# Performance work log

Measured on AMD Instinct MI355X. Metric: run time of the kernel, lower is better.

## Reference

```python
import jax, jax.numpy as jnp
import numpy as np


def _gcn_conv(h, src, dst, W, b, n):
    # PyG GCNConv: x @ W, then symmetric-normalized aggregation with self-loops
    deg = jax.ops.segment_sum(jnp.ones(src.shape[0], h.dtype), dst, num_segments=n)
    dinv = jax.lax.rsqrt(jnp.maximum(deg, 1.0))  # deg >= 1 because self-loops are included
    norm = dinv[src] * dinv[dst]                 # [E]
    m = (h @ W)[src] * norm[:, None]             # gather + scale
    return jax.ops.segment_sum(m, dst, num_segments=n) + b


def setup_inputs() -> dict:
    key = jax.random.key(0)
    N, E, F, H, L, V = 50000, 800000, 128, 256, 64, 128
    ks = jax.random.split(key, 16)
    s = lambda fan_in: 1.0 / np.sqrt(fan_in)
    return {
        "x": jax.random.randint(ks[0], (N,), 0, V),
        "edge_index": jax.random.randint(ks[1], (2, E), 0, N),
        "eps": jax.random.normal(ks[2], (N, L), jnp.float32),
        "emb": jax.random.normal(ks[3], (V, F), jnp.float32),
        "W1": jax.random.normal(ks[4], (F, H), jnp.float32) * s(F),
        "b1": jnp.zeros((H,), jnp.float32),
        "W2": jax.random.normal(ks[5], (H, H), jnp.float32) * s(H),
        "b2": jnp.zeros((H,), jnp.float32),
        "Wmu": jax.random.normal(ks[6], (H, L), jnp.float32) * s(H),
        "bmu": jnp.zeros((L,), jnp.float32),
        "Wlv": jax.random.normal(ks[7], (H, L), jnp.float32) * s(H),
        "blv": jnp.zeros((L,), jnp.float32),
        "W3": jax.random.normal(ks[8], (L, H), jnp.float32) * s(L),
        "b3": jnp.zeros((H,), jnp.float32),
        "W4": jax.random.normal(ks[9], (H, V), jnp.float32) * s(H),
        "b4": jnp.zeros((V,), jnp.float32),
        "Wcap": jax.random.normal(ks[10], (L, 1), jnp.float32) * s(L),
        "bcap": jnp.zeros((1,), jnp.float32),
    }


def reference(x, edge_index, eps, emb, W1, b1, W2, b2, Wmu, bmu, Wlv, blv, W3, b3, W4, b4, Wcap, bcap):
    n = x.shape[0]
    loops = jnp.arange(n, dtype=edge_index.dtype)
    src = jnp.concatenate([edge_index[0], loops])  # add self-loops once, reuse
    dst = jnp.concatenate([edge_index[1], loops])

    h = emb[x]                                      # [N, F] embedding lookup
    h = jax.nn.relu(_gcn_conv(h, src, dst, W1, b1, n))
    h = jax.nn.relu(_gcn_conv(h, src, dst, W2, b2, n))
    mu = h @ Wmu + bmu
    logvar = h @ Wlv + blv
    z = mu + eps * jnp.exp(0.5 * logvar)            # reparameterize
    recon_x = jax.nn.relu(z @ W3 + b3) @ W4 + b4    # decode
    capitalize = jax.nn.sigmoid(z @ Wcap + bcap)
    return recon_x, capitalize, mu, logvar
```

## Files before the change

### kernel.cpp

```cpp
#include <hip/hip_runtime.h>
#include <math.h>


typedef __attribute__((ext_vector_type(8))) short bf16x8;
typedef __attribute__((ext_vector_type(4))) float f32x4;

__device__ inline unsigned short f2bf(float x) {
    unsigned u = __float_as_uint(x);
    return (unsigned short)((u + 0x7FFFu + ((u >> 16) & 1u)) >> 16);
}
__device__ inline float bf2f(unsigned short h) {
    return __uint_as_float(((unsigned)h) << 16);
}

__global__ __launch_bounds__(256) void k_deg_count(const int* __restrict__ dst,
                                                   int* __restrict__ degint, int E) {
    int e = blockIdx.x * 256 + threadIdx.x;
    if (e < E) atomicAdd(&degint[dst[e]], 1);
}

#define SCAN_BLOCK 1024
__global__ __launch_bounds__(SCAN_BLOCK) void k_scan_local(
        const int* __restrict__ degint, int* __restrict__ row_ptr,
        int* __restrict__ bsum, float* __restrict__ dinv, int N) {
    __shared__ int s[SCAN_BLOCK];
    int gid = blockIdx.x * SCAN_BLOCK + threadIdx.x;
    int d = (gid < N) ? (degint[gid] + 1) : 0;
    if (gid < N) dinv[gid] = rsqrtf((float)d);
    s[threadIdx.x] = d;
    __syncthreads();
    for (int off = 1; off < SCAN_BLOCK; off <<= 1) {
        int t = (threadIdx.x >= off) ? s[threadIdx.x - off] : 0;
        __syncthreads();
        s[threadIdx.x] += t;
        __syncthreads();
    }
    if (gid < N) row_ptr[gid] = s[threadIdx.x] - d;
    if (threadIdx.x == SCAN_BLOCK - 1) bsum[blockIdx.x] = s[SCAN_BLOCK - 1];
}

__global__ void k_scan_bsum(int* __restrict__ bsum, int nb) {
    if (blockIdx.x == 0 && threadIdx.x == 0) {
        int acc = 0;
        for (int i = 0; i < nb; ++i) { int v = bsum[i]; bsum[i] = acc; acc += v; }
    }
}

__global__ __launch_bounds__(256) void k_scan_add(int* __restrict__ row_ptr,
                                                  const int* __restrict__ bsum,
                                                  int N, int T) {
    int gid = blockIdx.x * 256 + threadIdx.x;
    if (gid < N) row_ptr[gid] += bsum[gid / SCAN_BLOCK];
    if (gid == 0) row_ptr[N] = T;
}

__global__ __launch_bounds__(256) void k_fill(
        const int* __restrict__ src, const int* __restrict__ dst,
        const int* __restrict__ x, const float* __restrict__ dinv,
        const int* __restrict__ row_ptr, int* __restrict__ cursor,
        int4* __restrict__ pack, int E, int N) {
    const int base = (blockIdx.x * 256 + threadIdx.x) * 4;
#pragma unroll
    for (int j = 0; j < 4; ++j) {
        int e = base + j;
        if (e < E) {
            int s = src[e], d = dst[e];
            float w = dinv[s] * dinv[d];
            int pos = row_ptr[d] + atomicAdd(&cursor[d], 1);
            pack[pos] = make_int4(__float_as_int(w), x[s], s, 0);
        } else if (e < E + N) {
            int i = e - E;
            float di = dinv[i];
            int pos = row_ptr[i] + atomicAdd(&cursor[i], 1);
            pack[pos] = make_int4(__float_as_int(di * di), x[i], i, 0);
        }
    }
}

__global__ __launch_bounds__(256) void k_cvt_all(
        const float* __restrict__ B0, unsigned short* __restrict__ h0, int K0, int N0,
        const float* __restrict__ B1, unsigned short* __restrict__ h1, int K1, int N1,
        const float* __restrict__ B2, unsigned short* __restrict__ h2, int K2, int N2,
        const float* __restrict__ B3, unsigned short* __restrict__ h3, int K3, int N3,
        const float* __restrict__ B4, unsigned short* __restrict__ h4, int K4, int N4) {
    const float* B; unsigned short* Bh; int K, Ncol;
    switch (blockIdx.y) {
        case 0: B = B0; Bh = h0; K = K0; Ncol = N0; break;
        case 1: B = B1; Bh = h1; K = K1; Ncol = N1; break;
        case 2: B = B2; Bh = h2; K = K2; Ncol = N2; break;
        case 3: B = B3; Bh = h3; K = K3; Ncol = N3; break;
        default: B = B4; Bh = h4; K = K4; Ncol = N4; break;
    }
    int i = blockIdx.x * 256 + threadIdx.x;
    if (i >= K * Ncol) return;
    int k = i / Ncol, n = i - k * Ncol;
    Bh[(long)n * K + k] = f2bf(B[i]);
}

__global__ __launch_bounds__(256) void k_gemm_f32(
        const float* __restrict__ A, const float* __restrict__ B,
        unsigned short* __restrict__ Cb, int M, int K, int Ncol) {
    constexpr int BM = 64, BN = 64, BK = 16;
    __shared__ float As[BK][BM];
    __shared__ float Bs[BK][BN];
    const int tid = threadIdx.x;
    const int tx = tid & 15, ty = tid >> 4;
    const int rowBase = blockIdx.x * BM;
    const int colBase = blockIdx.y * BN;
    const int lr = tid >> 2, lc4 = tid & 3;
    const int br = tid >> 4, bc4 = tid & 15;
    const int arow = rowBase + lr;
    const int K4 = K >> 2, N4 = Ncol >> 2;
    const float4* A4 = (const float4*)A;
    const float4* B4 = (const float4*)B;
    float acc[4][4] = {{0.f}};
    for (int k0 = 0; k0 < K; k0 += BK) {
        float4 av = make_float4(0.f, 0.f, 0.f, 0.f);
        if (arow < M) av = A4[(long)arow * K4 + (k0 >> 2) + lc4];
        As[lc4 * 4 + 0][lr] = av.x;
        As[lc4 * 4 + 1][lr] = av.y;
        As[lc4 * 4 + 2][lr] = av.z;
        As[lc4 * 4 + 3][lr] = av.w;
        float4 bv = B4[(long)(k0 + br) * N4 + (colBase >> 2) + bc4];
        *(float4*)&Bs[br][bc4 * 4] = bv;
        __syncthreads();
#pragma unroll
        for (int k = 0; k < BK; ++k) {
            float4 a4v = *(const float4*)&As[k][ty * 4];
            float4 b4v = *(const float4*)&Bs[k][tx * 4];
            float aa[4] = {a4v.x, a4v.y, a4v.z, a4v.w};
            float bb[4] = {b4v.x, b4v.y, b4v.z, b4v.w};
#pragma unroll
            for (int i = 0; i < 4; ++i)
#pragma unroll
                for (int j = 0; j < 4; ++j)
                    acc[i][j] = fmaf(aa[i], bb[j], acc[i][j]);
        }
        __syncthreads();
    }
#pragma unroll
    for (int i = 0; i < 4; ++i) {
        int row = rowBase + ty * 4 + i;
        if (row < M) {
            ushort4 o;
            o.x = f2bf(acc[i][0]); o.y = f2bf(acc[i][1]);
            o.z = f2bf(acc[i][2]); o.w = f2bf(acc[i][3]);
            *(ushort4*)&Cb[(long)row * Ncol + colBase + tx * 4] = o;
        }
    }
}

template<bool RELU, bool BIAS, bool OUTBF>
__global__ __launch_bounds__(256) void k_gemm_mfma(
        const unsigned short* __restrict__ A, const unsigned short* __restrict__ Bt,
        const float* __restrict__ bias, float* __restrict__ Cf,
        unsigned short* __restrict__ Cb, int M, int K, int Ncol) {
    __shared__ unsigned short Ash[128][40];
    __shared__ unsigned short Bsh[64][40];
    const int tid = threadIdx.x;
    const int lane = tid & 63, w = tid >> 6;
    const int fr = lane & 15, quad = lane >> 4;
    const int wm0 = w * 32;
    const int rowBase = blockIdx.x * 128;
    const int colBase = blockIdx.y * 64;

    const int arow = tid >> 1;
    const int ahalf = (tid & 1) << 4;
    int agrow = rowBase + arow; if (agrow >= M) agrow = M - 1;
    const long abase = (long)agrow * K + ahalf;
    const int brow = tid >> 2;
    const int bseg = (tid & 3) << 3;
    const long bbase = (long)(colBase + brow) * K + bseg;

    f32x4 acc[2][4];
#pragma unroll
    for (int i = 0; i < 2; ++i)
#pragma unroll
        for (int j = 0; j < 4; ++j) acc[i][j] = (f32x4){0.f, 0.f, 0.f, 0.f};

    for (int k0 = 0; k0 < K; k0 += 32) {
        *(bf16x8*)&Ash[arow][ahalf]     = *(const bf16x8*)&A[abase + k0];
        *(bf16x8*)&Ash[arow][ahalf + 8] = *(const bf16x8*)&A[abase + k0 + 8];
        *(bf16x8*)&Bsh[brow][bseg]      = *(const bf16x8*)&Bt[bbase + k0];
        __syncthreads();
        bf16x8 ahf[2], bhf[4];
#pragma unroll
        for (int i = 0; i < 2; ++i)
            ahf[i] = *(const bf16x8*)&Ash[wm0 + i * 16 + fr][quad * 8];
#pragma unroll
        for (int j = 0; j < 4; ++j)
            bhf[j] = *(const bf16x8*)&Bsh[j * 16 + fr][quad * 8];
#pragma unroll
        for (int i = 0; i < 2; ++i)
#pragma unroll
            for (int j = 0; j < 4; ++j)
                acc[i][j] = __builtin_amdgcn_mfma_f32_16x16x32_bf16(
                    ahf[i], bhf[j], acc[i][j], 0, 0, 0);
        __syncthreads();
    }

#pragma unroll
    for (int i = 0; i < 2; ++i) {
        const int rowb = rowBase + wm0 + i * 16 + quad * 4;
#pragma unroll
        for (int j = 0; j < 4; ++j) {
            const int col = colBase + j * 16 + fr;
            const float bv = BIAS ? bias[col] : 0.f;
#pragma unroll
            for (int r = 0; r < 4; ++r) {
                const int row = rowb + r;
                if (row < M) {
                    float v = acc[i][j][r] + bv;
                    if (RELU) v = fmaxf(v, 0.f);
                    const long o = (long)row * Ncol + col;
                    if (OUTBF) Cb[o] = f2bf(v);
                    else       Cf[o] = v;
                }
            }
        }
    }
}

__global__ __launch_bounds__(256) void k_gemm_heads(
        const unsigned short* __restrict__ A, const unsigned short* __restrict__ Bt,
        const float* __restrict__ bmu, const float* __restrict__ blv,
        const float* __restrict__ eps, const float* __restrict__ Wcap,
        const float* __restrict__ bcap, float* __restrict__ mu,
        float* __restrict__ lv, unsigned short* __restrict__ Zh,
        float* __restrict__ cap, int M) {
    constexpr int K = 256;
    __shared__ unsigned short Ash[64][40];
    __shared__ unsigned short Bsh[128][40];
    const int tid = threadIdx.x;
    const int lane = tid & 63, w = tid >> 6;
    const int fr = lane & 15, quad = lane >> 4;
    const int wm0 = w * 16;
    const int rowBase = blockIdx.x * 64;

    const int arow = tid >> 2;
    const int aseg = (tid & 3) << 3;
    int agrow = rowBase + arow; if (agrow >= M) agrow = M - 1;
    const long abase = (long)agrow * K + aseg;
    const int brow = tid >> 1;
    const int bseg = (tid & 1) << 4;
    const long bbase = (long)brow * K + bseg;

    f32x4 acc[8];
#pragma unroll
    for (int j = 0; j < 8; ++j) acc[j] = (f32x4){0.f, 0.f, 0.f, 0.f};

    for (int k0 = 0; k0 < K; k0 += 32) {
        *(bf16x8*)&Ash[arow][aseg] = *(const bf16x8*)&A[abase + k0];
        *(bf16x8*)&Bsh[brow][bseg]     = *(const bf16x8*)&Bt[bbase + k0];
        *(bf16x8*)&Bsh[brow][bseg + 8] = *(const bf16x8*)&Bt[bbase + k0 + 8];
        __syncthreads();
        bf16x8 ahf = *(const bf16x8*)&Ash[wm0 + fr][quad * 8];
#pragma unroll
        for (int j = 0; j < 8; ++j) {
            bf16x8 bhf = *(const bf16x8*)&Bsh[j * 16 + fr][quad * 8];
            acc[j] = __builtin_amdgcn_mfma_f32_16x16x32_bf16(ahf, bhf, acc[j], 0, 0, 0);
        }
        __syncthreads();
    }

    float capacc[4] = {0.f, 0.f, 0.f, 0.f};
#pragma unroll
    for (int j = 0; j < 4; ++j) {
        const int c = j * 16 + fr;
        const float bm = bmu[c], bl = blv[c];
        const float wc = Wcap[c];
#pragma unroll
        for (int r = 0; r < 4; ++r) {
            const int row = rowBase + wm0 + quad * 4 + r;
            if (row < M) {
                const long o = (long)row * 64 + c;
                float mv = acc[j][r] + bm;
                float lvv = acc[j + 4][r] + bl;
                mu[o] = mv;
                lv[o] = lvv;
                float zz = fmaf(eps[o], expf(0.5f * lvv), mv);
                Zh[o] = f2bf(zz);
                capacc[r] = fmaf(zz, wc, capacc[r]);
            }
        }
    }
    const float b0 = bcap[0];
#pragma unroll
    for (int r = 0; r < 4; ++r) {
        float v = capacc[r];
        v += __shfl_xor(v, 1, 64);
        v += __shfl_xor(v, 2, 64);
        v += __shfl_xor(v, 4, 64);
        v += __shfl_xor(v, 8, 64);
        if (fr == 0) {
            const int row = rowBase + wm0 + quad * 4 + r;
            if (row < M) cap[row] = 1.f / (1.f + expf(-(v + b0)));
        }
    }
}

__global__ __launch_bounds__(256) void k_agg_tab(
        const unsigned short* __restrict__ tab, const int* __restrict__ row_ptr,
        const int4* __restrict__ pack, const float* __restrict__ bias,
        unsigned short* __restrict__ h1, int N) {
    const int wave = threadIdx.x >> 6;
    const int lane = threadIdx.x & 63;
    const int node = blockIdx.x * 4 + wave;
    if (node >= N) return;
    const ushort4* t4 = (const ushort4*)tab;
    float ax = 0.f, ay = 0.f, az = 0.f, aw = 0.f;
    const int beg = row_ptr[node], end = row_ptr[node + 1];
    int e = beg;
    for (; e + 4 <= end; e += 4) {
        int4 p0 = pack[e], p1 = pack[e + 1], p2 = pack[e + 2], p3 = pack[e + 3];
        ushort4 v0 = t4[(long)p0.y * 64 + lane];
        ushort4 v1 = t4[(long)p1.y * 64 + lane];
        ushort4 v2 = t4[(long)p2.y * 64 + lane];
        ushort4 v3 = t4[(long)p3.y * 64 + lane];
        float w0 = __int_as_float(p0.x), w1 = __int_as_float(p1.x);
        float w2 = __int_as_float(p2.x), w3 = __int_as_float(p3.x);
        ax = fmaf(bf2f(v0.x), w0, ax); ay = fmaf(bf2f(v0.y), w0, ay);
        az = fmaf(bf2f(v0.z), w0, az); aw = fmaf(bf2f(v0.w), w0, aw);
        ax = fmaf(bf2f(v1.x), w1, ax); ay = fmaf(bf2f(v1.y), w1, ay);
        az = fmaf(bf2f(v1.z), w1, az); aw = fmaf(bf2f(v1.w), w1, aw);
        ax = fmaf(bf2f(v2.x), w2, ax); ay = fmaf(bf2f(v2.y), w2, ay);
        az = fmaf(bf2f(v2.z), w2, az); aw = fmaf(bf2f(v2.w), w2, aw);
        ax = fmaf(bf2f(v3.x), w3, ax); ay = fmaf(bf2f(v3.y), w3, ay);
        az = fmaf(bf2f(v3.z), w3, az); aw = fmaf(bf2f(v3.w), w3, aw);
    }
    for (; e < end; ++e) {
        int4 p = pack[e];
        float w0 = __int_as_float(p.x);
        ushort4 v = t4[(long)p.y * 64 + lane];
        ax = fmaf(bf2f(v.x), w0, ax); ay = fmaf(bf2f(v.y), w0, ay);
        az = fmaf(bf2f(v.z), w0, az); aw = fmaf(bf2f(v.w), w0, aw);
    }
    float4 b = ((const float4*)bias)[lane];
    ax = fmaxf(ax + b.x, 0.f); ay = fmaxf(ay + b.y, 0.f);
    az = fmaxf(az + b.z, 0.f); aw = fmaxf(aw + b.w, 0.f);
    ushort4 o;
    o.x = f2bf(ax); o.y = f2bf(ay); o.z = f2bf(az); o.w = f2bf(aw);
    ((ushort4*)h1)[(long)node * 64 + lane] = o;
}

__global__ __launch_bounds__(256) void k_agg_nb(
        const unsigned short* __restrict__ h1, const int* __restrict__ row_ptr,
        const int4* __restrict__ pack, unsigned short* __restrict__ Ob, int N) {
    const int wave = threadIdx.x >> 6;
    const int lane = threadIdx.x & 63;
    const int node = blockIdx.x * 4 + wave;
    if (node >= N) return;
    const ushort4* h4 = (const ushort4*)h1;
    float ax = 0.f, ay = 0.f, az = 0.f, aw = 0.f;
    const int beg = row_ptr[node], end = row_ptr[node + 1];
    int e = beg;
    for (; e + 4 <= end; e += 4) {
        int4 p0 = pack[e], p1 = pack[e + 1], p2 = pack[e + 2], p3 = pack[e + 3];
        ushort4 v0 = h4[(long)p0.z * 64 + lane];
        ushort4 v1 = h4[(long)p1.z * 64 + lane];
        ushort4 v2 = h4[(long)p2.z * 64 + lane];
        ushort4 v3 = h4[(long)p3.z * 64 + lane];
        float w0 = __int_as_float(p0.x), w1 = __int_as_float(p1.x);
        float w2 = __int_as_float(p2.x), w3 = __int_as_float(p3.x);
        ax = fmaf(bf2f(v0.x), w0, ax); ay = fmaf(bf2f(v0.y), w0, ay);
        az = fmaf(bf2f(v0.z), w0, az); aw = fmaf(bf2f(v0.w), w0, aw);
        ax = fmaf(bf2f(v1.x), w1, ax); ay = fmaf(bf2f(v1.y), w1, ay);
        az = fmaf(bf2f(v1.z), w1, az); aw = fmaf(bf2f(v1.w), w1, aw);
        ax = fmaf(bf2f(v2.x), w2, ax); ay = fmaf(bf2f(v2.y), w2, ay);
        az = fmaf(bf2f(v2.z), w2, az); aw = fmaf(bf2f(v2.w), w2, aw);
        ax = fmaf(bf2f(v3.x), w3, ax); ay = fmaf(bf2f(v3.y), w3, ay);
        az = fmaf(bf2f(v3.z), w3, az); aw = fmaf(bf2f(v3.w), w3, aw);
    }
    for (; e < end; ++e) {
        int4 p = pack[e];
        float w0 = __int_as_float(p.x);
        ushort4 v = h4[(long)p.z * 64 + lane];
        ax = fmaf(bf2f(v.x), w0, ax); ay = fmaf(bf2f(v.y), w0, ay);
        az = fmaf(bf2f(v.z), w0, az); aw = fmaf(bf2f(v.w), w0, aw);
    }
    ushort4 o;
    o.x = f2bf(ax); o.y = f2bf(ay); o.z = f2bf(az); o.w = f2bf(aw);
    ((ushort4*)Ob)[(long)node * 64 + lane] = o;
}

extern "C" void kernel_launch(void* const* d_in, const int* in_sizes, int n_in,
                              void* d_out, int out_size, void* d_ws, size_t ws_size,
                              hipStream_t stream) {
    const int*   x    = (const int*)d_in[0];
    const int*   ei   = (const int*)d_in[1];
    const float* eps  = (const float*)d_in[2];
    const float* emb  = (const float*)d_in[3];
    const float* W1   = (const float*)d_in[4];
    const float* b1   = (const float*)d_in[5];
    const float* W2   = (const float*)d_in[6];
    const float* b2   = (const float*)d_in[7];
    const float* Wmu  = (const float*)d_in[8];
    const float* bmu  = (const float*)d_in[9];
    const float* Wlv  = (const float*)d_in[10];
    const float* blv  = (const float*)d_in[11];
    const float* W3   = (const float*)d_in[12];
    const float* b3   = (const float*)d_in[13];
    const float* W4   = (const float*)d_in[14];
    const float* b4   = (const float*)d_in[15];
    const float* Wcap = (const float*)d_in[16];
    const float* bcap = (const float*)d_in[17];

    const int N = in_sizes[0];
    const int E = in_sizes[1] / 2;
    const int H = in_sizes[5];
    const int L = in_sizes[9];
    const int V = in_sizes[15];
    const int F = in_sizes[4] / H;
    const int T = E + N;

    const int* src = ei;
    const int* dst = ei + E;

    char* w = (char*)d_ws;
    unsigned short* h1b  = (unsigned short*)w; w += (size_t)N * H * 2;
    unsigned short* a2b  = (unsigned short*)w; w += (size_t)N * H * 2;
    unsigned short* h2b  = (unsigned short*)w; w += (size_t)N * H * 2;
    unsigned short* zh   = (unsigned short*)w; w += (size_t)N * L * 2;
    int*   degint = (int*)w;   w += (size_t)N * 4;
    int*   cursor = (int*)w;   w += (size_t)N * 4;
    int*   rowp   = (int*)w;   w += (size_t)(N + 1) * 4;
    float* dinv   = (float*)w; w += (size_t)N * 4;
    int*   bsum   = (int*)w;   w += 256 * 4;
    int4*  pack   = (int4*)w;  w += (size_t)T * 16;
    unsigned short* tabH = (unsigned short*)w; w += (size_t)V * H * 2;
    unsigned short* W2t  = (unsigned short*)w; w += (size_t)H * H * 2;
    unsigned short* Wml  = (unsigned short*)w; w += (size_t)H * 2 * L * 2;
    unsigned short* W3t  = (unsigned short*)w; w += (size_t)L * H * 2;
    unsigned short* W4t  = (unsigned short*)w; w += (size_t)H * V * 2;

    unsigned short* tb = a2b;

    float* outp    = (float*)d_out;
    float* recon   = outp;
    float* cap     = outp + (size_t)N * V;
    float* mu      = outp + (size_t)N * V + N;
    float* logvar  = mu + (size_t)N * L;

    const int nN  = (N + 255) / 256;
    const int nE  = (E + 255) / 256;
    const int nT4 = (T + 1023) / 1024;
    const int nSc = (N + SCAN_BLOCK - 1) / SCAN_BLOCK;
    const int gM128 = (N + 127) / 128;
    const int gM64  = (N + 63) / 64;

    hipMemsetAsync(degint, 0, (size_t)N * 8, stream);
    k_deg_count<<<nE, 256, 0, stream>>>(dst, degint, E);
    k_scan_local<<<nSc, SCAN_BLOCK, 0, stream>>>(degint, rowp, bsum, dinv, N);
    k_scan_bsum<<<1, 64, 0, stream>>>(bsum, nSc);
    k_scan_add<<<nN, 256, 0, stream>>>(rowp, bsum, N, T);
    k_fill<<<nT4, 256, 0, stream>>>(src, dst, x, dinv, rowp, cursor, pack, E, N);

    k_cvt_all<<<dim3((H * H + 255) / 256, 5), 256, 0, stream>>>(
        W2, W2t, H, H,
        Wmu, Wml, H, L,
        Wlv, Wml + (size_t)L * H, H, L,
        W3, W3t, L, H,
        W4, W4t, H, V);

    k_gemm_f32<<<dim3(V / 64, H / 64), 256, 0, stream>>>(emb, W1, tabH, V, F, H);
    k_agg_tab<<<(N + 3) / 4, 256, 0, stream>>>(tabH, rowp, pack, b1, h1b, N);

    k_agg_nb<<<(N + 3) / 4, 256, 0, stream>>>(h1b, rowp, pack, a2b, N);
    k_gemm_mfma<true, true, true><<<dim3(gM128, H / 64), 256, 0, stream>>>(
        a2b, W2t, b2, nullptr, h2b, N, H, H);

    k_gemm_heads<<<gM64, 256, 0, stream>>>(
        h2b, Wml, bmu, blv, eps, Wcap, bcap, mu, logvar, zh, cap, N);

    k_gemm_mfma<true, true, true><<<dim3(gM128, H / 64), 256, 0, stream>>>(
        zh, W3t, b3, nullptr, tb, N, L, H);
    k_gemm_mfma<false, true, false><<<dim3(gM128, V / 64), 256, 0, stream>>>(
        tb, W4t, b4, recon, nullptr, N, H, V);
}
```

Before: 422.5 us.

## Replace first-layer table gather with token-count coefficient matrix times table GEMM

The first GCN layer is rewritten algebraically. Each node now builds a dense V-wide row of summed normalized edge weights per token (k_coef). That [N,V] bf16 matrix is multiplied by the transposed emb@W1 table using the MFMA GEMM, with bias and ReLU fused. This swaps a per-edge 256-wide gather for a per-edge 128-lane compare over the narrower pack fields plus a dense GEMM. In exchange it rounds the coefficients to bf16 and adds an N×V workspace buffer.

```diff
diff --git a/kernel.cpp b/kernel.cpp
--- a/kernel.cpp
+++ b/kernel.cpp
@@ -97,9 +97,9 @@
     Bh[(long)n * K + k] = f2bf(B[i]);
 }
 
-__global__ __launch_bounds__(256) void k_gemm_f32(
+__global__ __launch_bounds__(256) void k_gemm_f32t(
         const float* __restrict__ A, const float* __restrict__ B,
-        unsigned short* __restrict__ Cb, int M, int K, int Ncol) {
+        unsigned short* __restrict__ CbT, int M, int K, int Ncol) {
     constexpr int BM = 64, BN = 64, BK = 16;
     __shared__ float As[BK][BM];
     __shared__ float Bs[BK][BN];
@@ -142,12 +142,48 @@
     for (int i = 0; i < 4; ++i) {
         int row = rowBase + ty * 4 + i;
         if (row < M) {
-            ushort4 o;
-            o.x = f2bf(acc[i][0]); o.y = f2bf(acc[i][1]);
-            o.z = f2bf(acc[i][2]); o.w = f2bf(acc[i][3]);
-            *(ushort4*)&Cb[(long)row * Ncol + colBase + tx * 4] = o;
-        }
-    }
+#pragma unroll
+            for (int c = 0; c < 4; ++c) {
+                int col = colBase + tx * 4 + c;
+                CbT[(long)col * M + row] = f2bf(acc[i][c]);
+            }
+        }
+    }
+}
+
+__global__ __launch_bounds__(256) void k_coef(
+        const int4* __restrict__ pack, const int* __restrict__ row_ptr,
+        unsigned short* __restrict__ cb, int N) {
+    const int wave = threadIdx.x >> 6;
+    const int lane = threadIdx.x & 63;
+    const int node = blockIdx.x * 4 + wave;
+    if (node >= N) return;
+    const int tok0 = lane, tok1 = lane + 64;
+    float c0 = 0.f, c1 = 0.f;
+    const int beg = row_ptr[node], end = row_ptr[node + 1];
+    int e = beg;
+    for (; e + 4 <= end; e += 4) {
+        int2 p0 = *(const int2*)&pack[e];
+        int2 p1 = *(const int2*)&pack[e + 1];
+        int2 p2 = *(const int2*)&pack[e + 2];
+        int2 p3 = *(const int2*)&pack[e + 3];
+        c0 += (p0.y == tok0) ? __int_as_float(p0.x) : 0.f;
+        c1 += (p0.y == tok1) ? __int_as_float(p0.x) : 0.f;
+        c0 += (p1.y == tok0) ? __int_as_float(p1.x) : 0.f;
+        c1 += (p1.y == tok1) ? __int_as_float(p1.x) : 0.f;
+        c0 += (p2.y == tok0) ? __int_as_float(p2.x) : 0.f;
+        c1 += (p2.y == tok1) ? __int_as_float(p2.x) : 0.f;
+        c0 += (p3.y == tok0) ? __int_as_float(p3.x) : 0.f;
+        c1 += (p3.y == tok1) ? __int_as_float(p3.x) : 0.f;
+    }
+    for (; e < end; ++e) {
+        int2 p = *(const int2*)&pack[e];
+        c0 += (p.y == tok0) ? __int_as_float(p.x) : 0.f;
+        c1 += (p.y == tok1) ? __int_as_float(p.x) : 0.f;
+    }
+    const long base = (long)node * 128;
+    cb[base + lane]      = f2bf(c0);
+    cb[base + lane + 64] = f2bf(c1);
 }
 
 template<bool RELU, bool BIAS, bool OUTBF>
@@ -297,50 +333,6 @@
             if (row < M) cap[row] = 1.f / (1.f + expf(-(v + b0)));
         }
     }
-}
-
-__global__ __launch_bounds__(256) void k_agg_tab(
-        const unsigned short* __restrict__ tab, const int* __restrict__ row_ptr,
-        const int4* __restrict__ pack, const float* __restrict__ bias,
-        unsigned short* __restrict__ h1, int N) {
-    const int wave = threadIdx.x >> 6;
-    const int lane = threadIdx.x & 63;
-    const int node = blockIdx.x * 4 + wave;
-    if (node >= N) return;
-    const ushort4* t4 = (const ushort4*)tab;
-    float ax = 0.f, ay = 0.f, az = 0.f, aw = 0.f;
-    const int beg = row_ptr[node], end = row_ptr[node + 1];
-    int e = beg;
-    for (; e + 4 <= end; e += 4) {
-        int4 p0 = pack[e], p1 = pack[e + 1], p2 = pack[e + 2], p3 = pack[e + 3];
-        ushort4 v0 = t4[(long)p0.y * 64 + lane];
-        ushort4 v1 = t4[(long)p1.y * 64 + lane];
-        ushort4 v2 = t4[(long)p2.y * 64 + lane];
-        ushort4 v3 = t4[(long)p3.y * 64 + lane];
-        float w0 = __int_as_float(p0.x), w1 = __int_as_float(p1.x);
-        float w2 = __int_as_float(p2.x), w3 = __int_as_float(p3.x);
-        ax = fmaf(bf2f(v0.x), w0, ax); ay = fmaf(bf2f(v0.y), w0, ay);
-        az = fmaf(bf2f(v0.z), w0, az); aw = fmaf(bf2f(v0.w), w0, aw);
-        ax = fmaf(bf2f(v1.x), w1, ax); ay = fmaf(bf2f(v1.y), w1, ay);
-        az = fmaf(bf2f(v1.z), w1, az); aw = fmaf(bf2f(v1.w), w1, aw);
-        ax = fmaf(bf2f(v2.x), w2, ax); ay = fmaf(bf2f(v2.y), w2, ay);
-        az = fmaf(bf2f(v2.z), w2, az); aw = fmaf(bf2f(v2.w), w2, aw);
-        ax = fmaf(bf2f(v3.x), w3, ax); ay = fmaf(bf2f(v3.y), w3, ay);
-        az = fmaf(bf2f(v3.z), w3, az); aw = fmaf(bf2f(v3.w), w3, aw);
-    }
-    for (; e < end; ++e) {
-        int4 p = pack[e];
-        float w0 = __int_as_float(p.x);
-        ushort4 v = t4[(long)p.y * 64 + lane];
-        ax = fmaf(bf2f(v.x), w0, ax); ay = fmaf(bf2f(v.y), w0, ay);
-        az = fmaf(bf2f(v.z), w0, az); aw = fmaf(bf2f(v.w), w0, aw);
-    }
-    float4 b = ((const float4*)bias)[lane];
-    ax = fmaxf(ax + b.x, 0.f); ay = fmaxf(ay + b.y, 0.f);
-    az = fmaxf(az + b.z, 0.f); aw = fmaxf(aw + b.w, 0.f);
-    ushort4 o;
-    o.x = f2bf(ax); o.y = f2bf(ay); o.z = f2bf(az); o.w = f2bf(aw);
-    ((ushort4*)h1)[(long)node * 64 + lane] = o;
 }
 
 __global__ __launch_bounds__(256) void k_agg_nb(
@@ -421,13 +413,14 @@
     unsigned short* a2b  = (unsigned short*)w; w += (size_t)N * H * 2;
     unsigned short* h2b  = (unsigned short*)w; w += (size_t)N * H * 2;
     unsigned short* zh   = (unsigned short*)w; w += (size_t)N * L * 2;
+    unsigned short* cb   = (unsigned short*)w; w += (size_t)N * V * 2;
     int*   degint = (int*)w;   w += (size_t)N * 4;
     int*   cursor = (int*)w;   w += (size_t)N * 4;
     int*   rowp   = (int*)w;   w += (size_t)(N + 1) * 4;
     float* dinv   = (float*)w; w += (size_t)N * 4;
     int*   bsum   = (int*)w;   w += 256 * 4;
     int4*  pack   = (int4*)w;  w += (size_t)T * 16;
-    unsigned short* tabH = (unsigned short*)w; w += (size_t)V * H * 2;
+    unsigned short* tabT = (unsigned short*)w; w += (size_t)H * V * 2;
     unsigned short* W2t  = (unsigned short*)w; w += (size_t)H * H * 2;
     unsigned short* Wml  = (unsigned short*)w; w += (size_t)H * 2 * L * 2;
     unsigned short* W3t  = (unsigned short*)w; w += (size_t)L * H * 2;
@@ -462,8 +455,10 @@
         W3, W3t, L, H,
         W4, W4t, H, V);
 
-    k_gemm_f32<<<dim3(V / 64, H / 64), 256, 0, stream>>>(emb, W1, tabH, V, F, H);
-    k_agg_tab<<<(N + 3) / 4, 256, 0, stream>>>(tabH, rowp, pack, b1, h1b, N);
+    k_gemm_f32t<<<dim3(V / 64, H / 64), 256, 0, stream>>>(emb, W1, tabT, V, F, H);
+    k_coef<<<(N + 3) / 4, 256, 0, stream>>>(pack, rowp, cb, N);
+    k_gemm_mfma<true, true, true><<<dim3(gM128, H / 64), 256, 0, stream>>>(
+        cb, tabT, b1, nullptr, h1b, N, V, H);
 
     k_agg_nb<<<(N + 3) / 4, 256, 0, stream>>>(h1b, rowp, pack, a2b, N);
     k_gemm_mfma<true, true, true><<<dim3(gM128, H / 64), 256, 0, stream>>>(
```

New measurement: 416.8 us. No clear change (-1.3%).
